# Optimization experiments

Measured on AMD Instinct MI355X. Metric: run time of the kernel, lower is better.

Reference implementation:

```python
import jax, jax.numpy as jnp
import numpy as np
import math

POOLED_H = 2
POOLED_W = 64  # fixed: rois constructed so maxratio = POOLED_W / POOLED_H
NH = 256
NCLASS = 12  # len('0123456789.') + 1
C_IN = 512


def make_lstm_params(key, n_in, n_hidden):
    # torch nn.LSTM bidirectional: per direction W_ih [4H, in], W_hh [4H, H], b_ih, b_hh
    ks = jax.random.split(key, 8)
    s_i = 1.0 / np.sqrt(n_hidden)
    def u(k, shape):
        return jax.random.uniform(k, shape, jnp.float32, -s_i, s_i)
    p = {}
    for d, off in (('fw', 0), ('bw', 4)):
        p[d] = {
            'W_ih': u(ks[off + 0], (4 * n_hidden, n_in)),
            'W_hh': u(ks[off + 1], (4 * n_hidden, n_hidden)),
            'b_ih': u(ks[off + 2], (4 * n_hidden,)),
            'b_hh': u(ks[off + 3], (4 * n_hidden,)),
        }
    return p


def lstm_scan(x, p, n_hidden, reverse=False):
    # x: [T, B, n_in] -> [T, B, n_hidden]
    T, B, _ = x.shape
    W_ih, W_hh = p['W_ih'], p['W_hh']
    b = p['b_ih'] + p['b_hh']
    xg = jnp.einsum('tbi,gi->tbg', x, W_ih) + b  # [T,B,4H]

    def step(carry, xg_t):
        h, c = carry
        gates = xg_t + h @ W_hh.T
        i, f, g, o = jnp.split(gates, 4, axis=-1)
        i = jax.nn.sigmoid(i); f = jax.nn.sigmoid(f)
        g = jnp.tanh(g); o = jax.nn.sigmoid(o)
        c = f * c + i * g
        h = o * jnp.tanh(c)
        return (h, c), h

    h0 = jnp.zeros((B, n_hidden), x.dtype)
    c0 = jnp.zeros((B, n_hidden), x.dtype)
    _, hs = jax.lax.scan(step, (h0, c0), xg, reverse=reverse)
    return hs


def bilstm(x, p, n_hidden, W_emb, b_emb):
    hf = lstm_scan(x, p['fw'], n_hidden, reverse=False)
    hb = lstm_scan(x, p['bw'], n_hidden, reverse=True)
    h = jnp.concatenate([hf, hb], axis=-1)  # [T,B,2H]
    return h @ W_emb.T + b_emb


def roi_pool(base_feat, rois, pooled_h, pooled_w):
    # rois: [N,5] = [batch_idx, x1, y1, x2, y2] in feature coords (already scaled)
    # torch RoIPool: max pool over adaptive bins (spatial_scale=1).
    B, C, H, W = base_feat.shape

    def pool_one(roi):
        bi = roi[0].astype(jnp.int32)
        x1 = jnp.round(roi[1]).astype(jnp.int32)
        y1 = jnp.round(roi[2]).astype(jnp.int32)
        x2 = jnp.round(roi[3]).astype(jnp.int32)
        y2 = jnp.round(roi[4]).astype(jnp.int32)
        rw = jnp.maximum(x2 - x1 + 1, 1).astype(jnp.float32)
        rh = jnp.maximum(y2 - y1 + 1, 1).astype(jnp.float32)
        bin_h = rh / pooled_h
        bin_w = rw / pooled_w
        feat = base_feat[bi]  # [C,H,W]

        ph = jnp.arange(pooled_h)
        pw = jnp.arange(pooled_w)
        hstart = jnp.clip(jnp.floor(ph * bin_h).astype(jnp.int32) + y1, 0, H)
        hend = jnp.clip(jnp.ceil((ph + 1) * bin_h).astype(jnp.int32) + y1, 0, H)
        wstart = jnp.clip(jnp.floor(pw * bin_w).astype(jnp.int32) + x1, 0, W)
        wend = jnp.clip(jnp.ceil((pw + 1) * bin_w).astype(jnp.int32) + x1, 0, W)

        hh = jnp.arange(H)[None, :]
        ww = jnp.arange(W)[None, :]
        hmask = (hh >= hstart[:, None]) & (hh < hend[:, None])  # [ph,H]
        wmask = (ww >= wstart[:, None]) & (ww < wend[:, None])  # [pw,W]
        mask = hmask[:, None, :, None] & wmask[None, :, None, :]  # [ph,pw,H,W]
        neg = jnp.float32(-1e30)
        masked = jnp.where(mask[None], feat[:, None, None, :, :], neg)  # [C,ph,pw,H,W]
        pooled = masked.max(axis=(-2, -1))
        empty = ~mask.any(axis=(-2, -1))  # [ph,pw]
        return jnp.where(empty[None], 0.0, pooled)  # [C,ph,pw]

    return jax.vmap(pool_one)(rois)  # [N,C,ph,pw]


def setup_inputs() -> dict:
    key = jax.random.key(0)
    ks = jax.random.split(key, 10)
    B, C, H, W = 8, C_IN, 40, 160
    N = 32
    base_feat = jax.random.normal(ks[0], (B, C, H, W), jnp.float32)

    # rois normalized [bidx, x1, y1, x2, y2]; build so max aspect ratio = 32 -> pooled_w=64
    bidx = jax.random.randint(ks[1], (N,), 0, B).astype(jnp.float32)
    x1 = jax.random.uniform(ks[2], (N,), jnp.float32, 0.0, 0.3)
    y1 = jax.random.uniform(ks[3], (N,), jnp.float32, 0.0, 0.5)
    hgt = jax.random.uniform(ks[4], (N,), jnp.float32, 0.1, 0.3)
    # width/height ratio in normalized coords; after scaling by (W=160,H=40) feature
    # dims, ratio in feat coords = (w_n*160)/(h_n*40) = 4*w_n/h_n. Force max = 32.
    ratio = jax.random.uniform(ks[5], (N,), jnp.float32, 4.0, 32.0)
    ratio = ratio.at[0].set(32.0)
    wid_feat = ratio * (hgt * H)  # width in feature pixels
    wid = jnp.minimum(wid_feat / W, 0.99 - x1)
    # recompute so ratio exactly 32 at max: clamp keeps maxratio <= 32; pin roi 0
    wid = wid.at[0].set(jnp.minimum(32.0 * hgt[0] * H / W, 0.99 - x1[0]))
    hgt = hgt.at[0].set(wid[0] * W / (32.0 * H))
    x2 = x1 + wid
    y2 = jnp.minimum(y1 + hgt, 0.99)
    rois = jnp.stack([bidx, x1, y1, x2, y2], axis=1)

    text_length = jax.random.randint(ks[6], (1, N), 1, 8)
    text = jax.random.randint(ks[7], (1, 256), 1, NCLASS)  # labels 1..11

    # params
    p1 = make_lstm_params(ks[8], 1024, NH)
    p2 = make_lstm_params(ks[9], NH, NH)
    ke = jax.random.split(jax.random.key(1), 4)
    s1 = 1.0 / np.sqrt(2 * NH)
    W_emb1 = jax.random.uniform(ke[0], (NH, 2 * NH), jnp.float32, -s1, s1)
    b_emb1 = jax.random.uniform(ke[1], (NH,), jnp.float32, -s1, s1)
    W_emb2 = jax.random.uniform(ke[2], (NCLASS, 2 * NH), jnp.float32, -s1, s1)
    b_emb2 = jax.random.uniform(ke[3], (NCLASS,), jnp.float32, -s1, s1)

    params = {}
    for li, p in ((1, p1), (2, p2)):
        for d in ('fw', 'bw'):
            for n in ('W_ih', 'W_hh', 'b_ih', 'b_hh'):
                params[f'l{li}_{d}_{n}'] = p[d][n]
    params['W_emb1'] = W_emb1; params['b_emb1'] = b_emb1
    params['W_emb2'] = W_emb2; params['b_emb2'] = b_emb2

    return dict(base_feat=base_feat, text=text, text_length=text_length, rois=rois, **params)


def ctc_loss_sum(log_probs, labels, label_lengths):
    # log_probs: [T, B, K] log-softmax; labels: [B, Lmax] padded; blank = 0
    # standard CTC forward algorithm; returns sum of -log p over batch
    T, B, K = log_probs.shape
    Lmax = labels.shape[1]
    S = 2 * Lmax + 1
    # extended label sequence: blank, l1, blank, l2, ..., blank
    ext = jnp.zeros((B, S), jnp.int32)
    ext = ext.at[:, 1::2].set(labels.astype(jnp.int32))
    pos = jnp.arange(S)
    valid = pos[None, :] < (2 * label_lengths[:, None] + 1)

    # transition allowances
    same_as_2back = jnp.concatenate(
        [jnp.zeros((B, 2), bool), ext[:, 2:] == ext[:, :-2]], axis=1)
    is_blank = (ext == 0)
    allow_skip = (~is_blank) & (~same_as_2back)

    neg_inf = jnp.float32(-1e30)
    emit = jnp.take_along_axis(
        log_probs.transpose(1, 0, 2), ext[:, None, :].repeat(T, 1), axis=2
    ).transpose(1, 0, 2)  # [T, B, S]

    alpha0 = jnp.full((B, S), neg_inf)
    alpha0 = alpha0.at[:, 0].set(emit[0, :, 0])
    alpha0 = alpha0.at[:, 1].set(jnp.where(label_lengths > 0, emit[0, :, 1], neg_inf))

    def step(alpha, emit_t):
        a_prev1 = jnp.concatenate([jnp.full((B, 1), neg_inf), alpha[:, :-1]], axis=1)
        a_prev2 = jnp.concatenate([jnp.full((B, 2), neg_inf), alpha[:, :-2]], axis=1)
        a_prev2 = jnp.where(allow_skip, a_prev2, neg_inf)
        m = jnp.maximum(alpha, jnp.maximum(a_prev1, a_prev2))
        s = (jnp.exp(alpha - m) + jnp.exp(a_prev1 - m) + jnp.exp(a_prev2 - m))
        new = m + jnp.log(s) + emit_t
        new = jnp.where(valid, new, neg_inf)
        return new, None

    alpha_T, _ = jax.lax.scan(step, alpha0, emit[1:])
    end1 = 2 * label_lengths  # last blank
    end2 = 2 * label_lengths - 1  # last label
    aT1 = jnp.take_along_axis(alpha_T, end1[:, None], axis=1)[:, 0]
    aT2 = jnp.take_along_axis(alpha_T, jnp.maximum(end2, 0)[:, None], axis=1)[:, 0]
    aT2 = jnp.where(label_lengths > 0, aT2, neg_inf)
    m = jnp.maximum(aT1, aT2)
    logp = m + jnp.log(jnp.exp(aT1 - m) + jnp.exp(aT2 - m))
    return -jnp.sum(logp)


def reference(base_feat, text, text_length, rois,
              l1_fw_W_ih, l1_fw_W_hh, l1_fw_b_ih, l1_fw_b_hh,
              l1_bw_W_ih, l1_bw_W_hh, l1_bw_b_ih, l1_bw_b_hh,
              l2_fw_W_ih, l2_fw_W_hh, l2_fw_b_ih, l2_fw_b_hh,
              l2_bw_W_ih, l2_bw_W_hh, l2_bw_b_ih, l2_bw_b_hh,
              W_emb1, b_emb1, W_emb2, b_emb2):
    B, C, H, W = base_feat.shape
    rois = rois.at[:, jnp.array([1, 3])].multiply(W)
    rois = rois.at[:, jnp.array([2, 4])].multiply(H)
    pooled = roi_pool(base_feat, rois, POOLED_H, POOLED_W)  # [N,C,2,pw]
    N = pooled.shape[0]
    rnn_in = pooled.reshape(N, C * POOLED_H, POOLED_W).transpose(2, 0, 1)  # [T,N,1024]

    p1 = {'fw': dict(W_ih=l1_fw_W_ih, W_hh=l1_fw_W_hh, b_ih=l1_fw_b_ih, b_hh=l1_fw_b_hh),
          'bw': dict(W_ih=l1_bw_W_ih, W_hh=l1_bw_W_hh, b_ih=l1_bw_b_ih, b_hh=l1_bw_b_hh)}
    p2 = {'fw': dict(W_ih=l2_fw_W_ih, W_hh=l2_fw_W_hh, b_ih=l2_fw_b_ih, b_hh=l2_fw_b_hh),
          'bw': dict(W_ih=l2_bw_W_ih, W_hh=l2_bw_W_hh, b_ih=l2_bw_b_ih, b_hh=l2_bw_b_hh)}
    h1 = bilstm(rnn_in, p1, NH, W_emb1, b_emb1)
    preds = bilstm(h1, p2, NH, W_emb2, b_emb2)  # [T,N,nclass]

    log_probs = jax.nn.log_softmax(preds, axis=-1)
    tl = text_length[0].astype(jnp.int32)  # [N]
    # unflatten labels: text[0] holds concatenated labels; build padded [N, Lmax]
    Lmax = 8
    offsets = jnp.concatenate([jnp.zeros((1,), jnp.int32), jnp.cumsum(tl)[:-1]])
    idx = offsets[:, None] + jnp.arange(Lmax)[None, :]
    idx = jnp.clip(idx, 0, text.shape[1] - 1)
    labels = jnp.where(jnp.arange(Lmax)[None, :] < tl[:, None],
                       text[0][idx].astype(jnp.int32), 0)
    loss = ctc_loss_sum(log_probs, labels, tl) / N
    return loss
```

## Files before the change

### kernel.cpp

```cpp
#include <hip/hip_runtime.h>
#include <math.h>

#define TSTEPS 64
#define NSEQ   32
#define FH     40
#define FW     160

#define OFF_XGB    0u
#define OFF_RNNB   2097152u
#define OFF_W12B   3145728u
#define OFF_W22B   4194304u
#define OFF_WE1B   4456448u
#define OFF_WE2B   4521984u
#define OFF_PB1    4525056u
#define OFF_PB2    4527104u
#define OFF_W8L1F  4529152u
#define OFF_W8L1B  4594688u
#define OFF_W8L2F  4660224u
#define OFF_W8L2B  4725760u
#define OFF_HCB1   4791296u
#define OFF_HCB2   5315584u
#define OFF_H1B    5839872u
#define OFF_PREDS  6102016u

typedef __attribute__((ext_vector_type(8))) short short8;
typedef __attribute__((ext_vector_type(4))) float f32x4;
typedef __attribute__((ext_vector_type(4))) unsigned short ushort4v;
typedef __attribute__((ext_vector_type(4))) unsigned uint4v;

static __device__ inline unsigned short bf16c(float x) {
  union { float f; unsigned u; } v; v.f = x;
  unsigned r = v.u + 0x7fff + ((v.u >> 16) & 1);
  return (unsigned short)(r >> 16);
}
static __device__ inline float b2f(unsigned short u) {
  union { unsigned u; float f; } v; v.u = ((unsigned)u) << 16;
  return v.f;
}
static __device__ inline unsigned pk_bf16(float lo, float hi) {
  unsigned r;
  asm("v_cvt_pk_bf16_f32 %0, %1, %2" : "=v"(r) : "v"(lo), "v"(hi));
  return r;
}
static __device__ inline unsigned char fp8c(float x) {
  union { float f; unsigned u; } v; v.f = x;
  unsigned s = (v.u >> 24) & 0x80;
  float ax = fabsf(x);
  if (ax < 0.015625f) return (unsigned char)s;
  if (ax >= 448.0f) return (unsigned char)(s | 0x7e);
  unsigned e = (v.u >> 23) & 0xff;
  unsigned m = v.u & 0x7fffff;
  unsigned r = m + 0x7ffff + ((m >> 20) & 1);
  if (r >> 23) { e += 1; r = 0; }
  unsigned m3 = (r >> 20) & 7;
  int ee = (int)e - 127 + 7;
  if (ee > 15) return (unsigned char)(s | 0x7e);
  return (unsigned char)(s | (ee << 3) | m3);
}
static __device__ inline unsigned pk4_fp8(float a, float b, float c, float d) {
#if __has_builtin(__builtin_amdgcn_cvt_pk_fp8_f32)
  int r = __builtin_amdgcn_cvt_pk_fp8_f32(a, b, 0, false);
  r = __builtin_amdgcn_cvt_pk_fp8_f32(c, d, r, true);
  return (unsigned)r;
#else
  return (unsigned)fp8c(a) | ((unsigned)fp8c(b) << 8)
       | ((unsigned)fp8c(c) << 16) | ((unsigned)fp8c(d) << 24);
#endif
}

__global__ __launch_bounds__(256) void prep_kernel(
    const float* __restrict__ w1f, const float* __restrict__ w1b,
    const float* __restrict__ w2f, const float* __restrict__ w2b,
    const float* __restrict__ we1, const float* __restrict__ we2,
    const float* __restrict__ wh1f, const float* __restrict__ wh1b,
    const float* __restrict__ wh2f, const float* __restrict__ wh2b,
    const float* __restrict__ b1fi, const float* __restrict__ b1fh,
    const float* __restrict__ b1bi, const float* __restrict__ b1bh,
    const float* __restrict__ b2fi, const float* __restrict__ b2fh,
    const float* __restrict__ b2bi, const float* __restrict__ b2bh,
    const float* __restrict__ feat, const float* __restrict__ rois,
    unsigned short* __restrict__ w12b, unsigned short* __restrict__ w22b,
    unsigned short* __restrict__ we1o, unsigned short* __restrict__ we2o,
    unsigned char* __restrict__ o8l1f, unsigned char* __restrict__ o8l1b,
    unsigned char* __restrict__ o8l2f, unsigned char* __restrict__ o8l2b,
    float* __restrict__ pb1, float* __restrict__ pb2,
    unsigned short* __restrict__ rnn) {
  int b = blockIdx.x, tid = threadIdx.x;
  if (b < 2048) {
    const float* src = (b < 1024) ? w1f : w1b;
    unsigned short* dst = w12b + (size_t)((b < 1024) ? 0 : 1048576);
    int i = (b & 1023) * 256 + tid;
    int row = i >> 8, c4 = i & 255;
    int orow = (row & 255) * 4 + (row >> 8);
    float4 v = ((const float4*)src)[i];
    ushort4v o; o[0]=bf16c(v.x); o[1]=bf16c(v.y); o[2]=bf16c(v.z); o[3]=bf16c(v.w);
    *(ushort4v*)(dst + (size_t)orow * 1024 + c4 * 4) = o;
  } else if (b < 2560) {
    int bb = b - 2048;
    const float* src = (bb < 256) ? w2f : w2b;
    unsigned short* dst = w22b + (size_t)((bb < 256) ? 0 : 262144);
    int i = (bb & 255) * 256 + tid;
    int row = i >> 6, c4 = i & 63;
    int orow = (row & 255) * 4 + (row >> 8);
    float4 v = ((const float4*)src)[i];
    ushort4v o; o[0]=bf16c(v.x); o[1]=bf16c(v.y); o[2]=bf16c(v.z); o[3]=bf16c(v.w);
    *(ushort4v*)(dst + (size_t)orow * 256 + c4 * 4) = o;
  } else if (b < 2688) {
    int i = (b - 2560) * 256 + tid;
    int j = i >> 7, c4 = (i & 127) * 4;
    ushort4v o;
#pragma unroll
    for (int q = 0; q < 4; ++q) {
      int c = c4 + q;
      int d = c >> 8, k = c & 255;
      int u = (k >> 6) + (k & 63) * 4;
      o[q] = bf16c(we1[(size_t)j * 512 + d * 256 + u]);
    }
    ((ushort4v*)we1o)[i] = o;
  } else if (b < 2694) {
    int i = (b - 2688) * 256 + tid;
    int j = i >> 7, c4 = (i & 127) * 4;
    ushort4v o;
#pragma unroll
    for (int q = 0; q < 4; ++q) {
      int c = c4 + q;
      int d = c >> 8, k = c & 255;
      int u = (k >> 6) + (k & 63) * 4;
      o[q] = bf16c(we2[(size_t)j * 512 + d * 256 + u]);
    }
    ((ushort4v*)we2o)[i] = o;
  } else if (b < 3718) {
    int bb = b - 2694;
    int which = bb >> 8;
    const float* src = (which == 0) ? wh1f : (which == 1) ? wh1b
                     : (which == 2) ? wh2f : wh2b;
    unsigned char* dst = (which == 0) ? o8l1f : (which == 1) ? o8l1b
                       : (which == 2) ? o8l2f : o8l2b;
    int idx = (bb & 255) * 256 + tid;
    int row = idx >> 6, k4 = (idx & 63) * 4;
    const float* r = src + (size_t)row * 256;
    unsigned o = 0;
#pragma unroll
    for (int j = 0; j < 4; ++j) {
      int kp = k4 + j;
      int u = (kp >> 6) + (kp & 63) * 4;
      o |= ((unsigned)fp8c(r[u] * 64.0f)) << (8 * j);
    }
    ((unsigned*)dst)[idx] = o;
  } else if (b < 3726) {
    int m = (b - 3718) * 256 + tid;
    int dirq = m >> 10, mloc = m & 1023;
    int r = (mloc & 3) * 256 + (mloc >> 2);
    pb1[m] = dirq ? (b1bi[r] + b1bh[r]) : (b1fi[r] + b1fh[r]);
  } else if (b < 3734) {
    int m = (b - 3726) * 256 + tid;
    int dirq = m >> 10, mloc = m & 1023;
    int r = (mloc & 3) * 256 + (mloc >> 2);
    pb2[m] = dirq ? (b2bi[r] + b2bh[r]) : (b2fi[r] + b2fh[r]);
  } else {
    int b2 = b - 3734;
    int n = b2 >> 8, cg = b2 & 255;
    int pw = tid & 63, ph = (tid >> 6) & 1, cl = tid >> 7;
    int c = cg * 2 + cl;

    const float* r = rois + n * 5;
    int bi = (int)r[0];
    int x1 = (int)rintf(r[1] * (float)FW);
    int y1 = (int)rintf(r[2] * (float)FH);
    int x2 = (int)rintf(r[3] * (float)FW);
    int y2 = (int)rintf(r[4] * (float)FH);
    float rw = fmaxf((float)(x2 - x1 + 1), 1.0f);
    float rh = fmaxf((float)(y2 - y1 + 1), 1.0f);
    float bin_h = rh * 0.5f;
    float bin_w = rw * (1.0f / 64.0f);

    int hs = min(max((int)floorf((float)ph * bin_h) + y1, 0), FH);
    int he = min(max((int)ceilf((float)(ph + 1) * bin_h) + y1, 0), FH);
    int wst = min(max((int)floorf((float)pw * bin_w) + x1, 0), FW);
    int wen = min(max((int)ceilf((float)(pw + 1) * bin_w) + x1, 0), FW);

    float m = -1e30f;
    bool nonempty = (hs < he) && (wst < wen);
    const float* f = feat + ((size_t)bi * 512 + c) * (FH * FW);
    for (int h = hs; h < he; ++h) {
      const float* fr = f + h * FW;
      for (int w = wst; w < wen; ++w) m = fmaxf(m, fr[w]);
    }
    float out = nonempty ? m : 0.0f;
    rnn[((size_t)pw * NSEQ + n) * 1024 + c * 2 + ph] = bf16c(out);
  }
}

#define GPITCH 40
__global__ __launch_bounds__(256) void gemm_bf16(
    const unsigned short* __restrict__ A, const unsigned short* __restrict__ B,
    float* __restrict__ Cf, unsigned short* __restrict__ Cb,
    int M, int N, int K,
    const float* __restrict__ bm1, const float* __restrict__ bn, int mode) {
  __shared__ unsigned short Al[128 * GPITCH];
  __shared__ unsigned short Bl[128 * GPITCH];
  int m0 = blockIdx.y * 128, n0 = blockIdx.x * 128;
  int tid = threadIdx.x;
  int wid = tid >> 6, l = tid & 63, ln15 = l & 15, kg = l >> 4;
  int wm = wid >> 1, wn = wid & 1;

  f32x4 acc[4][4];
#pragma unroll
  for (int i = 0; i < 4; ++i)
#pragma unroll
    for (int j = 0; j < 4; ++j)
#pragma unroll
      for (int q = 0; q < 4; ++q) acc[i][j][q] = 0.0f;

  for (int k0 = 0; k0 < K; k0 += 32) {
#pragma unroll
    for (int it = 0; it < 2; ++it) {
      int chunk = tid + it * 256;
      int row = chunk >> 2, part = chunk & 3;
      short8 va = *(const short8*)(A + (size_t)(m0 + row) * K + k0 + part * 8);
      *(short8*)(Al + row * GPITCH + part * 8) = va;
      short8 vb;
      if (n0 + row < N) {
        vb = *(const short8*)(B + (size_t)(n0 + row) * K + k0 + part * 8);
      } else {
#pragma unroll
        for (int q = 0; q < 8; ++q) vb[q] = 0;
      }
      *(short8*)(Bl + row * GPITCH + part * 8) = vb;
    }
    __syncthreads();

    short8 a[4], b[4];
#pragma unroll
    for (int mt = 0; mt < 4; ++mt)
      a[mt] = *(const short8*)(Al + (wm * 64 + mt * 16 + ln15) * GPITCH + kg * 8);
#pragma unroll
    for (int nt = 0; nt < 4; ++nt)
      b[nt] = *(const short8*)(Bl + (wn * 64 + nt * 16 + ln15) * GPITCH + kg * 8);
#pragma unroll
    for (int mt = 0; mt < 4; ++mt)
#pragma unroll
      for (int nt = 0; nt < 4; ++nt)
        acc[mt][nt] = __builtin_amdgcn_mfma_f32_16x16x32_bf16(a[mt], b[nt], acc[mt][nt], 0, 0, 0);
    __syncthreads();
  }

  if (mode == 5) {
#pragma unroll
    for (int mt = 0; mt < 4; ++mt) {
      int mbase = m0 + wm * 64 + mt * 16 + kg * 4;
      f32x4 pbv = *(const f32x4*)(bm1 + mbase);
      int dirq = mbase >> 10;
      int unit = (mbase & 1023) >> 2;
#pragma unroll
      for (int nt = 0; nt < 4; ++nt) {
        int col = n0 + wn * 64 + nt * 16 + ln15;
        int t = col >> 5, n = col & 31;
        ushort4v q;
#pragma unroll
        for (int j = 0; j < 4; ++j)
          q[j] = bf16c((acc[mt][nt][j] + pbv[j]) * 1024.0f);
        *(ushort4v*)(Cb + (size_t)dirq * 2097152u + ((t << 8) + unit) * 128 + n * 4) = q;
      }
    }
    return;
  }

#pragma unroll
  for (int mt = 0; mt < 4; ++mt) {
#pragma unroll
    for (int j = 0; j < 4; ++j) {
      int m = m0 + wm * 64 + mt * 16 + kg * 4 + j;
      float bmv = bm1 ? bm1[m] : 0.0f;
#pragma unroll
      for (int nt = 0; nt < 4; ++nt) {
        int n = n0 + wn * 64 + nt * 16 + ln15;
        if (n < N) {
          float v = acc[mt][nt][j] + bmv;
          if (bn) v += bn[n];
          if (mode == 1) Cb[(size_t)m * N + n] = bf16c(v);
          else Cf[(size_t)m * N + n] = v;
        }
      }
    }
  }
}

__global__ __launch_bounds__(512, 2) void lstm_layer8(
    const unsigned short* __restrict__ xgb,
    const unsigned char* __restrict__ w8fw,
    const unsigned char* __restrict__ w8bw,
    unsigned short* __restrict__ hcatb) {
  const int dir = blockIdx.x >> 1;
  const int nbase = (blockIdx.x & 1) * 16;
  const int tid = threadIdx.x;
  const int w = tid >> 6;
  const int l = tid & 63;
  const int ln15 = l & 15;
  const int kg = l >> 4;
  const int u_wave = w * 32;

  __shared__ unsigned char h8[2][16][256];

  const unsigned char* W8 = dir ? w8bw : w8fw;

  unsigned long long afrag[8][8];
  {
    int gate = ln15 & 3, du = ln15 >> 2;
#pragma unroll
    for (int mt = 0; mt < 8; ++mt) {
      const unsigned char* wr = W8 + (size_t)((gate << 8) + u_wave + mt * 4 + du) * 256;
#pragma unroll
      for (int kc = 0; kc < 8; ++kc)
        afrag[mt][kc] = *(const unsigned long long*)(wr + kc * 32 + kg * 8);
    }
  }

  const unsigned short* xgd = xgb + (size_t)dir * 2097152u;
  const int lane_off = (nbase + ln15) * 4;
  float cst[8] = {0.f, 0.f, 0.f, 0.f, 0.f, 0.f, 0.f, 0.f};
  f32x4 acc[8];
  ushort4v xnext[8];

  {
    int t0 = dir ? 63 : 0;
    const unsigned short* xb = xgd + (size_t)t0 * 32768 + lane_off;
#pragma unroll
    for (int mt = 0; mt < 8; ++mt)
      xnext[mt] = *(const ushort4v*)(xb + (u_wave + mt * 4 + kg) * 128);
#pragma unroll
    for (int mt = 0; mt < 8; ++mt)
#pragma unroll
      for (int j = 0; j < 4; ++j) acc[mt][j] = b2f(xnext[mt][j]);
  }

  const int swzw = (ln15 & 7) << 4;
  const int myslot = kg * 64 + w * 8;
  const float kNI = -1.0f / 1024.0f;
  const float kP2 = 2.0f / 1024.0f;

  for (int s = 0; s < TSTEPS; ++s) {
    const int t = dir ? (63 - s) : s;
    const int p = s & 1;

    if (s < TSTEPS - 1) {
      int tn2 = dir ? (t - 1) : (t + 1);
      const unsigned short* xb = xgd + (size_t)tn2 * 32768 + lane_off;
#pragma unroll
      for (int mt = 0; mt < 8; ++mt)
        xnext[mt] = *(const ushort4v*)(xb + (u_wave + mt * 4 + kg) * 128);
    }

    if (s > 0) {
      const unsigned char* hrow = &h8[p][ln15][0];
#pragma unroll
      for (int kc = 0; kc < 8; ++kc) {
        unsigned long long hb =
            *(const unsigned long long*)(hrow + ((kc * 32 + kg * 8) ^ swzw));
#pragma unroll
        for (int mt = 0; mt < 8; ++mt)
          acc[mt] = __builtin_amdgcn_mfma_f32_16x16x32_fp8_fp8(
              (long)afrag[mt][kc], (long)hb, acc[mt], 0, 0, 0);
      }
    }

    {
      float hv[8];
#pragma unroll
      for (int mt = 0; mt < 8; ++mt) {
        float gi = __builtin_amdgcn_rcpf(1.0f + __expf(acc[mt][0] * kNI));
        float gf = __builtin_amdgcn_rcpf(1.0f + __expf(acc[mt][1] * kNI));
        float gg = 1.0f - 2.0f * __builtin_amdgcn_rcpf(1.0f + __expf(acc[mt][2] * kP2));
        float go = __builtin_amdgcn_rcpf(1.0f + __expf(acc[mt][3] * kNI));
        float c = gf * cst[mt] + gi * gg;
        cst[mt] = c;
        hv[mt] = go * (1.0f - 2.0f * __builtin_amdgcn_rcpf(1.0f + __expf(2.0f * c)));
      }
      unsigned d0 = pk4_fp8(hv[0] * 16.f, hv[1] * 16.f, hv[2] * 16.f, hv[3] * 16.f);
      unsigned d1 = pk4_fp8(hv[4] * 16.f, hv[5] * 16.f, hv[6] * 16.f, hv[7] * 16.f);
      unsigned long long pk = (unsigned long long)d0 | ((unsigned long long)d1 << 32);
      *(unsigned long long*)(&h8[p ^ 1][ln15][0] + (myslot ^ swzw)) = pk;

      uint4v hb16;
      hb16[0] = pk_bf16(hv[0], hv[1]);
      hb16[1] = pk_bf16(hv[2], hv[3]);
      hb16[2] = pk_bf16(hv[4], hv[5]);
      hb16[3] = pk_bf16(hv[6], hv[7]);
      *(uint4v*)(hcatb + ((size_t)t * NSEQ + nbase + ln15) * 512 + dir * 256 + myslot) = hb16;

      if (s < TSTEPS - 1) {
#pragma unroll
        for (int mt = 0; mt < 8; ++mt)
#pragma unroll
          for (int j = 0; j < 4; ++j) acc[mt][j] = b2f(xnext[mt][j]);
      }
    }

    __syncthreads();
  }
}

#define CTC_S 17
__global__ __launch_bounds__(576) void ctc_kernel(
    const float* __restrict__ preds,
    const int* __restrict__ text,
    const int* __restrict__ text_len,
    float* __restrict__ out) {
  __shared__ float lp[TSTEPS][NSEQ][12];
  __shared__ float alpha[2][NSEQ][CTC_S];
  __shared__ int ext[NSEQ][CTC_S];
  __shared__ unsigned char allow[NSEQ][CTC_S];
  __shared__ unsigned char validm[NSEQ][CTC_S];
  __shared__ int tlsh[NSEQ];
  __shared__ float logp_sh[NSEQ];

  int tid = threadIdx.x;

  for (int r = tid; r < TSTEPS * NSEQ; r += 576) {
    const float* p = preds + (size_t)r * 12;
    float mx = p[0];
#pragma unroll
    for (int k = 1; k < 12; ++k) mx = fmaxf(mx, p[k]);
    float ssum = 0.f;
#pragma unroll
    for (int k = 0; k < 12; ++k) ssum += __expf(p[k] - mx);
    float ls = mx + __logf(ssum);
    int t = r >> 5, b = r & 31;
#pragma unroll
    for (int k = 0; k < 12; ++k) lp[t][b][k] = p[k] - ls;
  }
  if (tid < NSEQ) tlsh[tid] = text_len[tid];
  __syncthreads();

  int b = tid & 31, sIdx = tid >> 5;
  bool active = sIdx < CTC_S;

  if (active) {
    int tl = tlsh[b];
    int off = 0;
    for (int i = 0; i < b; ++i) off += tlsh[i];
    int e = 0;
    if (sIdx & 1) {
      int lbl = (sIdx - 1) >> 1;
      int idx = off + lbl;
      if (idx > 255) idx = 255;
      e = (lbl < tl) ? text[idx] : 0;
    }
    ext[b][sIdx] = e;
    validm[b][sIdx] = (sIdx < 2 * tl + 1) ? 1 : 0;
  }
  __syncthreads();
  if (active) {
    int e = ext[b][sIdx];
    bool same2 = (sIdx >= 2) && (e == ext[b][sIdx - 2]);
    allow[b][sIdx] = ((sIdx >= 2) && (e != 0) && !same2) ? 1 : 0;
    float a = -1e30f;
    if (sIdx == 0) a = lp[0][b][0];
    else if (sIdx == 1 && tlsh[b] > 0) a = lp[0][b][ext[b][1]];
    alpha[0][b][sIdx] = a;
  }
  __syncthreads();

  for (int t = 1; t < TSTEPS; ++t) {
    int cur = (t - 1) & 1, nxt = t & 1;
    if (active) {
      float a = alpha[cur][b][sIdx];
      float a1 = (sIdx >= 1) ? alpha[cur][b][sIdx - 1] : -1e30f;
      float a2 = (sIdx >= 2 && allow[b][sIdx]) ? alpha[cur][b][sIdx - 2] : -1e30f;
      float m = fmaxf(a, fmaxf(a1, a2));
      float ssum = __expf(a - m) + __expf(a1 - m) + __expf(a2 - m);
      float nv = m + __logf(ssum) + lp[t][b][ext[b][sIdx]];
      alpha[nxt][b][sIdx] = validm[b][sIdx] ? nv : -1e30f;
    }
    __syncthreads();
  }

  if (tid < NSEQ) {
    int tl = tlsh[b];
    float a1 = alpha[1][b][2 * tl];
    float a2 = (tl > 0) ? alpha[1][b][2 * tl - 1] : -1e30f;
    float m = fmaxf(a1, a2);
    logp_sh[b] = m + __logf(__expf(a1 - m) + __expf(a2 - m));
  }
  __syncthreads();
  if (tid == 0) {
    float ssum = 0.f;
    for (int i = 0; i < NSEQ; ++i) ssum += logp_sh[i];
    out[0] = -ssum / (float)NSEQ;
  }
}

extern "C" void kernel_launch(void* const* d_in, const int* in_sizes, int n_in,
                              void* d_out, int out_size, void* d_ws, size_t ws_size,
                              hipStream_t stream) {
  (void)in_sizes; (void)n_in; (void)out_size; (void)ws_size;
  const float* base_feat = (const float*)d_in[0];
  const int* text = (const int*)d_in[1];
  const int* text_len = (const int*)d_in[2];
  const float* rois = (const float*)d_in[3];
  const float* l1_fw_W_ih = (const float*)d_in[4];
  const float* l1_fw_W_hh = (const float*)d_in[5];
  const float* l1_fw_b_ih = (const float*)d_in[6];
  const float* l1_fw_b_hh = (const float*)d_in[7];
  const float* l1_bw_W_ih = (const float*)d_in[8];
  const float* l1_bw_W_hh = (const float*)d_in[9];
  const float* l1_bw_b_ih = (const float*)d_in[10];
  const float* l1_bw_b_hh = (const float*)d_in[11];
  const float* l2_fw_W_ih = (const float*)d_in[12];
  const float* l2_fw_W_hh = (const float*)d_in[13];
  const float* l2_fw_b_ih = (const float*)d_in[14];
  const float* l2_fw_b_hh = (const float*)d_in[15];
  const float* l2_bw_W_ih = (const float*)d_in[16];
  const float* l2_bw_W_hh = (const float*)d_in[17];
  const float* l2_bw_b_ih = (const float*)d_in[18];
  const float* l2_bw_b_hh = (const float*)d_in[19];
  const float* W_emb1 = (const float*)d_in[20];
  const float* b_emb1 = (const float*)d_in[21];
  const float* W_emb2 = (const float*)d_in[22];
  const float* b_emb2 = (const float*)d_in[23];

  float* ws = (float*)d_ws;
  unsigned short* xgb  = (unsigned short*)(ws + OFF_XGB);
  unsigned short* rnnb = (unsigned short*)(ws + OFF_RNNB);
  unsigned short* w12b = (unsigned short*)(ws + OFF_W12B);
  unsigned short* w22b = (unsigned short*)(ws + OFF_W22B);
  unsigned short* we1b = (unsigned short*)(ws + OFF_WE1B);
  unsigned short* we2b = (unsigned short*)(ws + OFF_WE2B);
  float* pb1 = ws + OFF_PB1;
  float* pb2 = ws + OFF_PB2;
  unsigned char* w8l1f = (unsigned char*)(ws + OFF_W8L1F);
  unsigned char* w8l1b = (unsigned char*)(ws + OFF_W8L1B);
  unsigned char* w8l2f = (unsigned char*)(ws + OFF_W8L2F);
  unsigned char* w8l2b = (unsigned char*)(ws + OFF_W8L2B);
  unsigned short* hcb1 = (unsigned short*)(ws + OFF_HCB1);
  unsigned short* hcb2 = (unsigned short*)(ws + OFF_HCB2);
  unsigned short* h1b  = (unsigned short*)(ws + OFF_H1B);
  float* preds = ws + OFF_PREDS;

  prep_kernel<<<11926, 256, 0, stream>>>(
      l1_fw_W_ih, l1_bw_W_ih, l2_fw_W_ih, l2_bw_W_ih, W_emb1, W_emb2,
      l1_fw_W_hh, l1_bw_W_hh, l2_fw_W_hh, l2_bw_W_hh,
      l1_fw_b_ih, l1_fw_b_hh, l1_bw_b_ih, l1_bw_b_hh,
      l2_fw_b_ih, l2_fw_b_hh, l2_bw_b_ih, l2_bw_b_hh,
      base_feat, rois,
      w12b, w22b, we1b, we2b, w8l1f, w8l1b, w8l2f, w8l2b, pb1, pb2, rnnb);

  gemm_bf16<<<dim3(16, 16), 256, 0, stream>>>(w12b, rnnb, nullptr, xgb,
      2048, 2048, 1024, pb1, nullptr, 5);

  lstm_layer8<<<4, 512, 0, stream>>>(xgb, w8l1f, w8l1b, hcb1);

  gemm_bf16<<<dim3(2, 16), 256, 0, stream>>>(hcb1, we1b, nullptr, h1b,
      2048, 256, 512, nullptr, b_emb1, 1);

  gemm_bf16<<<dim3(16, 16), 256, 0, stream>>>(w22b, h1b, nullptr, xgb,
      2048, 2048, 256, pb2, nullptr, 5);

  lstm_layer8<<<4, 512, 0, stream>>>(xgb, w8l2f, w8l2b, hcb2);

  gemm_bf16<<<dim3(1, 16), 256, 0, stream>>>(hcb2, we2b, preds, nullptr,
      2048, 12, 512, nullptr, b_emb2, 0);

  ctc_kernel<<<1, 576, 0, stream>>>(preds, text, text_len, (float*)d_out);
}
```

Before: 446.5 us.

## Keep CTC alpha in registers via wave shuffles; halve GEMM N-tile for more blocks

The CTC forward recursion now places each sequence's 17 states in half a wavefront. The alpha values stay in registers and neighbours are read with lane shuffles, which removes the block-wide __syncthreads on every time step. The kernel now runs 1024 threads, two sequences per wave. Separately, the bf16 GEMM N-tile drops from 128 to 64, doubling the grid so more CUs are busy, at the cost of less reuse of the A tile.

```diff
diff --git a/kernel.cpp b/kernel.cpp
--- a/kernel.cpp
+++ b/kernel.cpp
@@ -198,17 +198,17 @@
     int M, int N, int K,
     const float* __restrict__ bm1, const float* __restrict__ bn, int mode) {
   __shared__ unsigned short Al[128 * GPITCH];
-  __shared__ unsigned short Bl[128 * GPITCH];
-  int m0 = blockIdx.y * 128, n0 = blockIdx.x * 128;
+  __shared__ unsigned short Bl[64 * GPITCH];
+  int m0 = blockIdx.y * 128, n0 = blockIdx.x * 64;
   int tid = threadIdx.x;
   int wid = tid >> 6, l = tid & 63, ln15 = l & 15, kg = l >> 4;
   int wm = wid >> 1, wn = wid & 1;
 
-  f32x4 acc[4][4];
+  f32x4 acc[4][2];
 #pragma unroll
   for (int i = 0; i < 4; ++i)
 #pragma unroll
-    for (int j = 0; j < 4; ++j)
+    for (int j = 0; j < 2; ++j)
 #pragma unroll
       for (int q = 0; q < 4; ++q) acc[i][j][q] = 0.0f;
 
@@ -219,6 +219,9 @@
       int row = chunk >> 2, part = chunk & 3;
       short8 va = *(const short8*)(A + (size_t)(m0 + row) * K + k0 + part * 8);
       *(short8*)(Al + row * GPITCH + part * 8) = va;
+    }
+    {
+      int row = tid >> 2, part = tid & 3;
       short8 vb;
       if (n0 + row < N) {
         vb = *(const short8*)(B + (size_t)(n0 + row) * K + k0 + part * 8);
@@ -230,17 +233,17 @@
     }
     __syncthreads();
 
-    short8 a[4], b[4];
+    short8 a[4], b[2];
 #pragma unroll
     for (int mt = 0; mt < 4; ++mt)
       a[mt] = *(const short8*)(Al + (wm * 64 + mt * 16 + ln15) * GPITCH + kg * 8);
 #pragma unroll
-    for (int nt = 0; nt < 4; ++nt)
-      b[nt] = *(const short8*)(Bl + (wn * 64 + nt * 16 + ln15) * GPITCH + kg * 8);
+    for (int nt = 0; nt < 2; ++nt)
+      b[nt] = *(const short8*)(Bl + (wn * 32 + nt * 16 + ln15) * GPITCH + kg * 8);
 #pragma unroll
     for (int mt = 0; mt < 4; ++mt)
 #pragma unroll
-      for (int nt = 0; nt < 4; ++nt)
+      for (int nt = 0; nt < 2; ++nt)
         acc[mt][nt] = __builtin_amdgcn_mfma_f32_16x16x32_bf16(a[mt], b[nt], acc[mt][nt], 0, 0, 0);
     __syncthreads();
   }
@@ -253,8 +256,8 @@
       int dirq = mbase >> 10;
       int unit = (mbase & 1023) >> 2;
 #pragma unroll
-      for (int nt = 0; nt < 4; ++nt) {
-        int col = n0 + wn * 64 + nt * 16 + ln15;
+      for (int nt = 0; nt < 2; ++nt) {
+        int col = n0 + wn * 32 + nt * 16 + ln15;
         int t = col >> 5, n = col & 31;
         ushort4v q;
 #pragma unroll
@@ -273,8 +276,8 @@
       int m = m0 + wm * 64 + mt * 16 + kg * 4 + j;
       float bmv = bm1 ? bm1[m] : 0.0f;
 #pragma unroll
-      for (int nt = 0; nt < 4; ++nt) {
-        int n = n0 + wn * 64 + nt * 16 + ln15;
+      for (int nt = 0; nt < 2; ++nt) {
+        int n = n0 + wn * 32 + nt * 16 + ln15;
         if (n < N) {
           float v = acc[mt][nt][j] + bmv;
           if (bn) v += bn[n];
@@ -401,22 +404,19 @@
 }
 
 #define CTC_S 17
-__global__ __launch_bounds__(576) void ctc_kernel(
+__global__ __launch_bounds__(1024) void ctc_kernel(
     const float* __restrict__ preds,
     const int* __restrict__ text,
     const int* __restrict__ text_len,
     float* __restrict__ out) {
   __shared__ float lp[TSTEPS][NSEQ][12];
-  __shared__ float alpha[2][NSEQ][CTC_S];
-  __shared__ int ext[NSEQ][CTC_S];
-  __shared__ unsigned char allow[NSEQ][CTC_S];
-  __shared__ unsigned char validm[NSEQ][CTC_S];
   __shared__ int tlsh[NSEQ];
+  __shared__ float alpha_f[NSEQ][CTC_S];
   __shared__ float logp_sh[NSEQ];
 
   int tid = threadIdx.x;
 
-  for (int r = tid; r < TSTEPS * NSEQ; r += 576) {
+  for (int r = tid; r < TSTEPS * NSEQ; r += 1024) {
     const float* p = preds + (size_t)r * 12;
     float mx = p[0];
 #pragma unroll
@@ -432,55 +432,52 @@
   if (tid < NSEQ) tlsh[tid] = text_len[tid];
   __syncthreads();
 
-  int b = tid & 31, sIdx = tid >> 5;
-  bool active = sIdx < CTC_S;
-
-  if (active) {
-    int tl = tlsh[b];
+  const int wv = tid >> 6;
+  const int lane = tid & 63;
+  const int b = wv * 2 + (lane >> 5);
+  const int s = lane & 31;
+  const bool active = (s < CTC_S);
+
+  int tl = tlsh[b];
+  int e = 0;
+  if (active && (s & 1)) {
     int off = 0;
     for (int i = 0; i < b; ++i) off += tlsh[i];
-    int e = 0;
-    if (sIdx & 1) {
-      int lbl = (sIdx - 1) >> 1;
-      int idx = off + lbl;
-      if (idx > 255) idx = 255;
-      e = (lbl < tl) ? text[idx] : 0;
-    }
-    ext[b][sIdx] = e;
-    validm[b][sIdx] = (sIdx < 2 * tl + 1) ? 1 : 0;
-  }
+    int lbl = (s - 1) >> 1;
+    int idx = off + lbl;
+    if (idx > 255) idx = 255;
+    e = (lbl < tl) ? text[idx] : 0;
+  }
+  int e2 = __shfl_up(e, 2, 32);
+  bool allow = active && (s >= 2) && (e != 0) && (e != e2);
+  bool valid = active && (s < 2 * tl + 1);
+
+  float alpha = -1e30f;
+  if (active) {
+    if (s == 0) alpha = lp[0][b][0];
+    else if (s == 1 && tl > 0) alpha = lp[0][b][e];
+  }
+
+  for (int t = 1; t < TSTEPS; ++t) {
+    float a1 = __shfl_up(alpha, 1, 32);
+    float a2 = __shfl_up(alpha, 2, 32);
+    if (s < 1) a1 = -1e30f;
+    if (!allow) a2 = -1e30f;
+    float m = fmaxf(alpha, fmaxf(a1, a2));
+    float ssum = __expf(alpha - m) + __expf(a1 - m) + __expf(a2 - m);
+    float nv = m + __logf(ssum) + lp[t][b][e];
+    alpha = valid ? nv : -1e30f;
+  }
+
+  if (active) alpha_f[b][s] = alpha;
   __syncthreads();
-  if (active) {
-    int e = ext[b][sIdx];
-    bool same2 = (sIdx >= 2) && (e == ext[b][sIdx - 2]);
-    allow[b][sIdx] = ((sIdx >= 2) && (e != 0) && !same2) ? 1 : 0;
-    float a = -1e30f;
-    if (sIdx == 0) a = lp[0][b][0];
-    else if (sIdx == 1 && tlsh[b] > 0) a = lp[0][b][ext[b][1]];
-    alpha[0][b][sIdx] = a;
-  }
-  __syncthreads();
-
-  for (int t = 1; t < TSTEPS; ++t) {
-    int cur = (t - 1) & 1, nxt = t & 1;
-    if (active) {
-      float a = alpha[cur][b][sIdx];
-      float a1 = (sIdx >= 1) ? alpha[cur][b][sIdx - 1] : -1e30f;
-      float a2 = (sIdx >= 2 && allow[b][sIdx]) ? alpha[cur][b][sIdx - 2] : -1e30f;
-      float m = fmaxf(a, fmaxf(a1, a2));
-      float ssum = __expf(a - m) + __expf(a1 - m) + __expf(a2 - m);
-      float nv = m + __logf(ssum) + lp[t][b][ext[b][sIdx]];
-      alpha[nxt][b][sIdx] = validm[b][sIdx] ? nv : -1e30f;
-    }
-    __syncthreads();
-  }
 
   if (tid < NSEQ) {
-    int tl = tlsh[b];
-    float a1 = alpha[1][b][2 * tl];
-    float a2 = (tl > 0) ? alpha[1][b][2 * tl - 1] : -1e30f;
+    int tl2 = tlsh[tid];
+    float a1 = alpha_f[tid][2 * tl2];
+    float a2 = (tl2 > 0) ? alpha_f[tid][2 * tl2 - 1] : -1e30f;
     float m = fmaxf(a1, a2);
-    logp_sh[b] = m + __logf(__expf(a1 - m) + __expf(a2 - m));
+    logp_sh[tid] = m + __logf(__expf(a1 - m) + __expf(a2 - m));
   }
   __syncthreads();
   if (tid == 0) {
@@ -545,15 +542,15 @@
       base_feat, rois,
       w12b, w22b, we1b, we2b, w8l1f, w8l1b, w8l2f, w8l2b, pb1, pb2, rnnb);
 
-  gemm_bf16<<<dim3(16, 16), 256, 0, stream>>>(w12b, rnnb, nullptr, xgb,
+  gemm_bf16<<<dim3(32, 16), 256, 0, stream>>>(w12b, rnnb, nullptr, xgb,
       2048, 2048, 1024, pb1, nullptr, 5);
 
   lstm_layer8<<<4, 512, 0, stream>>>(xgb, w8l1f, w8l1b, hcb1);
 
-  gemm_bf16<<<dim3(2, 16), 256, 0, stream>>>(hcb1, we1b, nullptr, h1b,
+  gemm_bf16<<<dim3(4, 16), 256, 0, stream>>>(hcb1, we1b, nullptr, h1b,
       2048, 256, 512, nullptr, b_emb1, 1);
 
-  gemm_bf16<<<dim3(16, 16), 256, 0, stream>>>(w22b, h1b, nullptr, xgb,
+  gemm_bf16<<<dim3(32, 16), 256, 0, stream>>>(w22b, h1b, nullptr, xgb,
       2048, 2048, 256, pb2, nullptr, 5);
 
   lstm_layer8<<<4, 512, 0, stream>>>(xgb, w8l2f, w8l2b, hcb2);
@@ -561,5 +558,5 @@
   gemm_bf16<<<dim3(1, 16), 256, 0, stream>>>(hcb2, we2b, preds, nullptr,
       2048, 12, 512, nullptr, b_emb2, 0);
 
-  ctc_kernel<<<1, 576, 0, stream>>>(preds, text, text_len, (float*)d_out);
-}
+  ctc_kernel<<<1, 1024, 0, stream>>>(preds, text, text_len, (float*)d_out);
+}
```

Result: faster. 419.8 us, median of 2 (-6.0%).
